# Performance work log

Hardware: AMD Instinct MI355X
Metric: run time of the kernel (lower is better)

## Reference

```python
import jax, jax.numpy as jnp
import numpy as np

N_STATIC = 20
N_DYNAMIC = 10
INPUT_DIM = N_STATIC + N_DYNAMIC * 9 + 8  # 118
EMBED = 128
HIDDEN = 1536
HIDDEN2 = 1024
OUT = 128
T = 2048


def setup_inputs() -> dict:
    key = jax.random.key(0)
    ks = jax.random.split(key, 20)
    s = lambda i, shape: jax.random.normal(ks[i], shape, dtype=jnp.float32) * 0.02
    inp = {
        "inputVecs": jax.random.normal(ks[0], (T, INPUT_DIM), dtype=jnp.float32),
        # init_hidden(): randn(num_layers, 1, hidden_dim) -> stored as [2, H]
        "h0": jax.random.normal(ks[1], (2, HIDDEN), dtype=jnp.float32),
        "c0": jax.random.normal(ks[2], (2, HIDDEN), dtype=jnp.float32),
        # LSTM layer 0 (input = INPUT_DIM + EMBED)
        "W_ih0": s(3, (4 * HIDDEN, INPUT_DIM + EMBED)),
        "W_hh0": s(4, (4 * HIDDEN, HIDDEN)),
        "b_ih0": s(5, (4 * HIDDEN,)),
        "b_hh0": s(6, (4 * HIDDEN,)),
        # LSTM layer 1
        "W_ih1": s(7, (4 * HIDDEN, HIDDEN)),
        "W_hh1": s(8, (4 * HIDDEN, HIDDEN)),
        "b_ih1": s(9, (4 * HIDDEN,)),
        "b_hh1": s(10, (4 * HIDDEN,)),
        # hiddenLinear: hidden_dim -> hidden2
        "W_hl": s(11, (HIDDEN2, HIDDEN)),
        "b_hl": s(12, (HIDDEN2,)),
        # linear: hidden2 -> output_dim
        "W_out": s(13, (OUT, HIDDEN2)),
        "b_out": s(14, (OUT,)),
        # map: output_dim -> embed_size
        "W_map": s(15, (EMBED, OUT)),
        "b_map": s(16, (EMBED,)),
    }
    return inp


def _lstm_cell(x, h, c, W_ih, W_hh, b_ih, b_hh):
    # torch gate order: i, f, g, o
    gates = W_ih @ x + b_ih + W_hh @ h + b_hh
    i, f, g, o = jnp.split(gates, 4)
    i = jax.nn.sigmoid(i)
    f = jax.nn.sigmoid(f)
    g = jnp.tanh(g)
    o = jax.nn.sigmoid(o)
    c_new = f * c + i * g
    h_new = o * jnp.tanh(c_new)
    return h_new, c_new


def reference(inputVecs, h0, c0, W_ih0, W_hh0, b_ih0, b_hh0,
              W_ih1, W_hh1, b_ih1, b_hh1,
              W_hl, b_hl, W_out, b_out, W_map, b_map):
    embed0 = jnp.zeros((EMBED,), dtype=inputVecs.dtype)

    def step(carry, x):
        h, c, emb = carry  # h,c: [2, H]; emb: [EMBED]
        xt = jnp.concatenate([x, emb])
        h0n, c0n = _lstm_cell(xt, h[0], c[0], W_ih0, W_hh0, b_ih0, b_hh0)
        h1n, c1n = _lstm_cell(h0n, h[1], c[1], W_ih1, W_hh1, b_ih1, b_hh1)
        # dropout p=0 -> identity; two stacked linears (no nonlinearity, faithful)
        y = W_out @ (W_hl @ h1n + b_hl) + b_out
        y = jax.nn.softmax(y)
        emb_new = W_map @ y + b_map
        return (jnp.stack([h0n, h1n]), jnp.stack([c0n, c1n]), emb_new), y

    _, outputs = jax.lax.scan(step, (h0, c0, embed0), inputVecs)
    return outputs  # [T, OUT]
```

## Files before the change

kernel.cpp:

```cpp
#include <hip/hip_runtime.h>
#include <math.h>
#include <stdint.h>

#define T_STEPS 2048
#define XDIM 118
#define EMBD 128
#define HD 1536
#define NA 96
#define NB 128
#define NBLK (NA + NB + 1)

#define EP_A   0
#define EP_B   128
#define EP_C   256
#define EP_AG  288
#define EP_N   320

#define SMEM_BYTES 160032

struct Params {
  const float *x, *h0in, *c0in;
  const float *Wih0, *Whh0, *bih0, *bhh0;
  const float *Wih1, *Whh1, *bih1, *bhh1;
  const float *Whl, *bhl, *Wout, *bout, *Wmap, *bmap;
  float *PRE, *Wc, *bc, *h0buf, *h1buf, *embbuf, *PART;
  uint32_t *ep;
  float *out;
};

__device__ __forceinline__ float bf_lo(uint32_t u){ return __uint_as_float(u << 16); }
__device__ __forceinline__ float bf_hi(uint32_t u){ return __uint_as_float(u & 0xffff0000u); }
__device__ __forceinline__ uint32_t packbf(float a, float b){
  uint32_t ua = __float_as_uint(a), ub = __float_as_uint(b);
  ua = (ua + 0x7fffu + ((ua >> 16) & 1u)) >> 16;
  ub = (ub + 0x7fffu + ((ub >> 16) & 1u)) & 0xffff0000u;
  return (ua & 0xffffu) | ub;
}
__device__ __forceinline__ float gload(const float* p){
  return __hip_atomic_load(p, __ATOMIC_RELAXED, __HIP_MEMORY_SCOPE_AGENT);
}
__device__ __forceinline__ void gstore(float* p, float v){
  __hip_atomic_store(p, v, __ATOMIC_RELAXED, __HIP_MEMORY_SCOPE_AGENT);
}
__device__ __forceinline__ uint32_t gloadu(const uint32_t* p){
  return __hip_atomic_load(p, __ATOMIC_RELAXED, __HIP_MEMORY_SCOPE_AGENT);
}
__device__ __forceinline__ void gstoreu(uint32_t* p, uint32_t v){
  __hip_atomic_store(p, v, __ATOMIC_RELAXED, __HIP_MEMORY_SCOPE_AGENT);
}
__device__ __forceinline__ float sigm(float x){ return 1.f / (1.f + __expf(-x)); }

__device__ __forceinline__ float asrc(const Params& P, int r, int k){
  if (k < HD) return P.Whh0[(size_t)r * HD + k];
  return P.Wih0[(size_t)r * (XDIM + EMBD) + XDIM + (k - HD)];
}
__device__ void run_A(const Params& P, int bid, uint32_t* smem){
  const int tid = threadIdx.x;
  const int w = tid >> 6, l = tid & 63;
  const int O = bid * 16 + w;
  float* xv = (float*)smem;
  uint2* wl2 = (uint2*)(smem + 1664);
  uint32_t wr[4][8];
  uint32_t wremb[4];
#pragma unroll
  for (int g = 0; g < 4; ++g){
    int r = g * HD + O;
#pragma unroll
    for (int p = 0; p < 8; ++p)
      wr[g][p] = packbf(asrc(P, r, 128 * p + 2 * l), asrc(P, r, 128 * p + 2 * l + 1));
#pragma unroll
    for (int q = 0; q < 2; ++q){
      uint2 u;
      u.x = packbf(asrc(P, r, 128 * (8 + 2 * q) + 2 * l), asrc(P, r, 128 * (8 + 2 * q) + 2 * l + 1));
      u.y = packbf(asrc(P, r, 128 * (9 + 2 * q) + 2 * l), asrc(P, r, 128 * (9 + 2 * q) + 2 * l + 1));
      wl2[(q * 4 + g) * 1024 + tid] = u;
    }
    wremb[g] = packbf(asrc(P, r, 1536 + 2 * l), asrc(P, r, 1537 + 2 * l));
  }
  float cst = P.c0in[O];
  int alive = 1;
  __syncthreads();
  for (int t = 0; t < T_STEPS; ++t){
    const float* pre = P.PRE + (size_t)t * 6144;
    float q0 = pre[O], q1 = pre[HD + O], q2 = pre[2 * HD + O], q3 = pre[3 * HD + O];
    if (w == 0 && alive){
      uint32_t n = 0;
      while (gloadu(P.ep + EP_AG) < (uint32_t)t){
        if (++n > 5000000u){ alive = 0; break; }
      }
    }
    __syncthreads();
    const float* hp = P.h0buf + (((t & 1) ^ 1) * HD);
    xv[tid] = gload(hp + tid);
    if (tid < 512) xv[1024 + tid] = gload(hp + 1024 + tid);
    __syncthreads();
    float a0 = 0.f, a1 = 0.f, a2 = 0.f, a3 = 0.f;
#pragma unroll
    for (int p = 0; p < 8; ++p){
      float2 x2 = *(const float2*)&xv[128 * p + 2 * l];
      uint32_t u0 = wr[0][p], u1 = wr[1][p], u2 = wr[2][p], u3 = wr[3][p];
      a0 += bf_lo(u0) * x2.x + bf_hi(u0) * x2.y;
      a1 += bf_lo(u1) * x2.x + bf_hi(u1) * x2.y;
      a2 += bf_lo(u2) * x2.x + bf_hi(u2) * x2.y;
      a3 += bf_lo(u3) * x2.x + bf_hi(u3) * x2.y;
    }
#pragma unroll
    for (int q = 0; q < 2; ++q){
      float2 xa = *(const float2*)&xv[128 * (8 + 2 * q) + 2 * l];
      float2 xb = *(const float2*)&xv[128 * (9 + 2 * q) + 2 * l];
      uint2 u0 = wl2[(q * 4 + 0) * 1024 + tid];
      uint2 u1 = wl2[(q * 4 + 1) * 1024 + tid];
      uint2 u2 = wl2[(q * 4 + 2) * 1024 + tid];
      uint2 u3 = wl2[(q * 4 + 3) * 1024 + tid];
      a0 += bf_lo(u0.x) * xa.x + bf_hi(u0.x) * xa.y + bf_lo(u0.y) * xb.x + bf_hi(u0.y) * xb.y;
      a1 += bf_lo(u1.x) * xa.x + bf_hi(u1.x) * xa.y + bf_lo(u1.y) * xb.x + bf_hi(u1.y) * xb.y;
      a2 += bf_lo(u2.x) * xa.x + bf_hi(u2.x) * xa.y + bf_lo(u2.y) * xb.x + bf_hi(u2.y) * xb.y;
      a3 += bf_lo(u3.x) * xa.x + bf_hi(u3.x) * xa.y + bf_lo(u3.y) * xb.x + bf_hi(u3.y) * xb.y;
    }
    if (w == 0 && alive){
      uint32_t n = 0;
      while (gloadu(P.ep + EP_C) < (uint32_t)t){
        if (++n > 5000000u){ alive = 0; break; }
      }
    }
    __syncthreads();
    if (tid < EMBD) xv[HD + tid] = gload(P.embbuf + (((t & 1) ^ 1) * EMBD) + tid);
    __syncthreads();
    {
      float2 x2 = *(const float2*)&xv[1536 + 2 * l];
      a0 += bf_lo(wremb[0]) * x2.x + bf_hi(wremb[0]) * x2.y;
      a1 += bf_lo(wremb[1]) * x2.x + bf_hi(wremb[1]) * x2.y;
      a2 += bf_lo(wremb[2]) * x2.x + bf_hi(wremb[2]) * x2.y;
      a3 += bf_lo(wremb[3]) * x2.x + bf_hi(wremb[3]) * x2.y;
    }
#pragma unroll
    for (int m = 1; m < 64; m <<= 1){
      a0 += __shfl_xor(a0, m, 64);
      a1 += __shfl_xor(a1, m, 64);
      a2 += __shfl_xor(a2, m, 64);
      a3 += __shfl_xor(a3, m, 64);
    }
    float gi = sigm(a0 + q0);
    float gf = sigm(a1 + q1);
    float gg = tanhf(a2 + q2);
    float go = sigm(a3 + q3);
    cst = gf * cst + gi * gg;
    float hn = go * tanhf(cst);
    if (l == 0) gstore(P.h0buf + (t & 1) * HD + O, hn);
    __syncthreads();
    if (tid == 0) gstoreu(P.ep + EP_A + bid, (uint32_t)(t + 1));
  }
}

__device__ __forceinline__ float bsrc(const Params& P, int r, int k){
  if (k < HD) return P.Wih1[(size_t)r * HD + k];
  return P.Whh1[(size_t)r * HD + (k - HD)];
}
__device__ void run_B(const Params& P, int bidb, uint32_t* smem){
  const int tid = threadIdx.x;
  const int w = tid >> 6, l = tid & 63;
  const int base = bidb * 12;
  float* xv = (float*)smem;
  uint2* wl2 = (uint2*)(smem + 3072);
  float* g1lds = (float*)(smem + 39936);
  float* c1lds = g1lds + 48;
  float* h1lds = c1lds + 12;
  uint32_t wr[3][12];
  float bias[3];
#pragma unroll
  for (int jj = 0; jj < 3; ++jj){
    int idx = 3 * w + jj;
    int g = idx / 12, o = idx % 12;
    int r = g * HD + base + o;
    bias[jj] = P.bih1[r] + P.bhh1[r];
#pragma unroll
    for (int p = 0; p < 12; ++p)
      wr[jj][p] = packbf(bsrc(P, r, 128 * p + 2 * l), bsrc(P, r, 128 * p + 2 * l + 1));
#pragma unroll
    for (int q = 0; q < 6; ++q){
      uint2 u;
      u.x = packbf(bsrc(P, r, 128 * (12 + 2 * q) + 2 * l), bsrc(P, r, 128 * (12 + 2 * q) + 2 * l + 1));
      u.y = packbf(bsrc(P, r, 128 * (13 + 2 * q) + 2 * l), bsrc(P, r, 128 * (13 + 2 * q) + 2 * l + 1));
      wl2[(q * 3 + jj) * 1024 + tid] = u;
    }
  }
  const int jrow = tid >> 2, cpart = tid & 3;
  float wc0 = 0.f, wc1 = 0.f, wc2 = 0.f;
  if (tid < 512){
    const float* wcp = P.Wc + (size_t)jrow * HD + base + cpart * 3;
    wc0 = wcp[0]; wc1 = wcp[1]; wc2 = wcp[2];
  }
  if (tid < 12) c1lds[tid] = P.c0in[HD + base + tid];
  int alive = 1;
  __syncthreads();
  for (int t = 0; t < T_STEPS; ++t){
    if (w == 0 && alive){
      uint32_t n = 0;
      while (gloadu(P.ep + EP_C) < (uint32_t)t){
        if (++n > 5000000u){ alive = 0; break; }
      }
    }
    __syncthreads();
    const float* h1p = P.h1buf + (((t & 1) ^ 1) * HD);
    xv[1536 + tid] = gload(h1p + tid);
    if (tid < 512) xv[2560 + tid] = gload(h1p + 1024 + tid);
    __syncthreads();
    float a0 = 0.f, a1 = 0.f, a2 = 0.f;
#pragma unroll
    for (int q = 0; q < 6; ++q){
      float2 xa = *(const float2*)&xv[128 * (12 + 2 * q) + 2 * l];
      float2 xb = *(const float2*)&xv[128 * (13 + 2 * q) + 2 * l];
      uint2 u0 = wl2[(q * 3 + 0) * 1024 + tid];
      uint2 u1 = wl2[(q * 3 + 1) * 1024 + tid];
      uint2 u2 = wl2[(q * 3 + 2) * 1024 + tid];
      a0 += bf_lo(u0.x) * xa.x + bf_hi(u0.x) * xa.y + bf_lo(u0.y) * xb.x + bf_hi(u0.y) * xb.y;
      a1 += bf_lo(u1.x) * xa.x + bf_hi(u1.x) * xa.y + bf_lo(u1.y) * xb.x + bf_hi(u1.y) * xb.y;
      a2 += bf_lo(u2.x) * xa.x + bf_hi(u2.x) * xa.y + bf_lo(u2.y) * xb.x + bf_hi(u2.y) * xb.y;
    }
    if (w == 0 && alive){
      uint32_t tgt = (uint32_t)(t + 1), n = 0;
      if (bidb == 0){
        while (1){
          uint32_t v0 = gloadu(P.ep + EP_A + l);
          uint32_t v1 = (l < 32) ? gloadu(P.ep + EP_A + 64 + l) : tgt;
          if (__all(v0 >= tgt && v1 >= tgt)) break;
          if (++n > 5000000u){ alive = 0; break; }
        }
        if (l == 0 && alive) gstoreu(P.ep + EP_AG, tgt);
      } else {
        while (gloadu(P.ep + EP_AG) < tgt){
          if (++n > 5000000u){ alive = 0; break; }
        }
      }
    }
    __syncthreads();
    const float* h0p = P.h0buf + (t & 1) * HD;
    xv[tid] = gload(h0p + tid);
    if (tid < 512) xv[1024 + tid] = gload(h0p + 1024 + tid);
    __syncthreads();
#pragma unroll
    for (int p = 0; p < 12; ++p){
      float2 x2 = *(const float2*)&xv[128 * p + 2 * l];
      uint32_t u0 = wr[0][p], u1 = wr[1][p], u2 = wr[2][p];
      a0 += bf_lo(u0) * x2.x + bf_hi(u0) * x2.y;
      a1 += bf_lo(u1) * x2.x + bf_hi(u1) * x2.y;
      a2 += bf_lo(u2) * x2.x + bf_hi(u2) * x2.y;
    }
#pragma unroll
    for (int m = 1; m < 64; m <<= 1){
      a0 += __shfl_xor(a0, m, 64);
      a1 += __shfl_xor(a1, m, 64);
      a2 += __shfl_xor(a2, m, 64);
    }
    if (l == 0){
      g1lds[3 * w + 0] = a0 + bias[0];
      g1lds[3 * w + 1] = a1 + bias[1];
      g1lds[3 * w + 2] = a2 + bias[2];
    }
    __syncthreads();
    if (tid < 12){
      int o = tid;
      float gi = sigm(g1lds[o]);
      float gf = sigm(g1lds[12 + o]);
      float gg = tanhf(g1lds[24 + o]);
      float go = sigm(g1lds[36 + o]);
      float c = gf * c1lds[o] + gi * gg;
      c1lds[o] = c;
      float hn = go * tanhf(c);
      h1lds[o] = hn;
      gstore(P.h1buf + (t & 1) * HD + base + o, hn);
    }
    __syncthreads();
    if (tid < 512){
      float pp = wc0 * h1lds[cpart * 3] + wc1 * h1lds[cpart * 3 + 1] + wc2 * h1lds[cpart * 3 + 2];
      pp += __shfl_xor(pp, 1, 64);
      pp += __shfl_xor(pp, 2, 64);
      if (cpart == 0) gstore(P.PART + bidb * 128 + jrow, pp);
    }
    __syncthreads();
    if (tid == 0) gstoreu(P.ep + EP_B + bidb, (uint32_t)(t + 1));
  }
}

__device__ void run_C(const Params& P, uint32_t* smem){
  const int tid = threadIdx.x;
  float* partred = (float*)smem;
  float* lg   = (float*)(smem + 1024);
  float* plds = (float*)(smem + 1152);
  float* bcs  = (float*)(smem + 1280);
  float* red2 = (float*)(smem + 1408);
  float wm[16];
  const int e = tid >> 3, jc = tid & 7;
#pragma unroll
  for (int i = 0; i < 16; ++i) wm[i] = P.Wmap[(size_t)e * 128 + jc * 16 + i];
  float bm = P.bmap[e];
  if (tid < 128) bcs[tid] = P.bc[tid];
  int alive = 1;
  const int w = tid >> 6, l = tid & 63;
  __syncthreads();
  for (int t = 0; t < T_STEPS; ++t){
    if (w == 0 && alive){
      uint32_t tgt = (uint32_t)(t + 1), n = 0;
      while (1){
        uint32_t v0 = gloadu(P.ep + EP_B + l);
        uint32_t v1 = gloadu(P.ep + EP_B + 64 + l);
        if (__all(v0 >= tgt && v1 >= tgt)) break;
        if (++n > 5000000u){ alive = 0; break; }
      }
    }
    __syncthreads();
    const int j = tid & 127, b8 = tid >> 7;
    float s = 0.f;
#pragma unroll
    for (int i = 0; i < 16; ++i) s += gload(P.PART + (b8 * 16 + i) * 128 + j);
    partred[b8 * 128 + j] = s;
    __syncthreads();
    if (tid < 128){
      float lt = bcs[tid];
#pragma unroll
      for (int i = 0; i < 8; ++i) lt += partred[i * 128 + tid];
      lg[tid] = lt;
    }
    __syncthreads();
    if (tid < 64){
      float m = fmaxf(lg[tid], lg[tid + 64]);
#pragma unroll
      for (int k = 1; k < 64; k <<= 1) m = fmaxf(m, __shfl_xor(m, k, 64));
      float sd = __expf(lg[tid] - m) + __expf(lg[tid + 64] - m);
#pragma unroll
      for (int k = 1; k < 64; k <<= 1) sd += __shfl_xor(sd, k, 64);
      if (tid == 0){ red2[0] = m; red2[1] = 1.f / sd; }
    }
    __syncthreads();
    if (tid < 128){
      float pv = __expf(lg[tid] - red2[0]) * red2[1];
      plds[tid] = pv;
      P.out[(size_t)t * 128 + tid] = pv;
    }
    __syncthreads();
    float a = 0.f;
#pragma unroll
    for (int i = 0; i < 16; ++i) a += wm[i] * plds[jc * 16 + i];
    a += __shfl_xor(a, 1, 64);
    a += __shfl_xor(a, 2, 64);
    a += __shfl_xor(a, 4, 64);
    if (jc == 0) gstore(P.embbuf + (t & 1) * EMBD + e, a + bm);
    __syncthreads();
    if (tid == 0) gstoreu(P.ep + EP_C, (uint32_t)(t + 1));
  }
}

__global__ __launch_bounds__(1024) void k_lstm(Params P){
  extern __shared__ __align__(16) uint32_t smem[];
  int bid = blockIdx.x;
  if (bid < NA) run_A(P, bid, smem);
  else if (bid < NA + NB) run_B(P, bid - NA, smem);
  else run_C(P, smem);
}

__global__ void k_init(const float* h0in, float* h0buf, float* h1buf, float* embbuf,
                       uint32_t* ep){
  int tid = threadIdx.x;
  for (int i = tid; i < HD; i += 256){
    float a = h0in[i], b = h0in[HD + i];
    h0buf[i] = a; h0buf[HD + i] = a;
    h1buf[i] = b; h1buf[HD + i] = b;
  }
  if (tid < 128){ embbuf[tid] = 0.f; embbuf[128 + tid] = 0.f; }
  for (int i = tid; i < EP_N; i += 256) ep[i] = 0u;
}

__global__ void k_pre(const float* x, const float* Wih0, const float* bih0, const float* bhh0, float* PRE){
  int tb = blockIdx.x >> 2;
  int rc = blockIdx.x & 3;
  int tid = threadIdx.x;
  __shared__ float xl[32 * XDIM];
  for (int i = tid; i < 32 * XDIM; i += 256){
    int tt = i / XDIM, k = i % XDIM;
    xl[i] = x[(size_t)(tb * 32 + tt) * XDIM + k];
  }
  __syncthreads();
  for (int rr = 0; rr < 6; ++rr){
    int r = rc * HD + rr * 256 + tid;
    float acc[32];
#pragma unroll
    for (int t = 0; t < 32; ++t) acc[t] = 0.f;
    const float* wrow = Wih0 + (size_t)r * (XDIM + EMBD);
    for (int k = 0; k < XDIM; ++k){
      float wv = wrow[k];
#pragma unroll
      for (int t = 0; t < 32; ++t) acc[t] += wv * xl[t * XDIM + k];
    }
    float bb = bih0[r] + bhh0[r];
    for (int t = 0; t < 32; ++t)
      PRE[(size_t)(tb * 32 + t) * 6144 + r] = acc[t] + bb;
  }
}

__global__ void k_wc(const float* Whl, const float* Wout, const float* bhl, const float* bout,
                     float* Wc, float* bc){
  if (blockIdx.x == 96){
    int j = threadIdx.x;
    if (j < 128){
      float a = 0.f;
      for (int m = 0; m < 1024; ++m) a += Wout[(size_t)j * 1024 + m] * bhl[m];
      bc[j] = a + bout[j];
    }
    return;
  }
  int kt = blockIdx.x % 6, jt = blockIdx.x / 6;
  __shared__ float wo[8 * 1024];
  int tid = threadIdx.x;
  for (int i = tid; i < 8 * 1024; i += 256) wo[i] = Wout[(size_t)(jt * 8) * 1024 + i];
  __syncthreads();
  int k = kt * 256 + tid;
  float acc[8];
#pragma unroll
  for (int jj = 0; jj < 8; ++jj) acc[jj] = 0.f;
  for (int m = 0; m < 1024; ++m){
    float wl = Whl[(size_t)m * HD + k];
#pragma unroll
    for (int jj = 0; jj < 8; ++jj) acc[jj] += wo[jj * 1024 + m] * wl;
  }
#pragma unroll
  for (int jj = 0; jj < 8; ++jj) Wc[(size_t)(jt * 8 + jj) * HD + k] = acc[jj];
}

__global__ void k_sentinel(float* out){ out[0] = 1.0e6f; }

extern "C" void kernel_launch(void* const* d_in, const int* in_sizes, int n_in,
                              void* d_out, int out_size, void* d_ws, size_t ws_size,
                              hipStream_t stream){
  (void)in_sizes; (void)n_in; (void)out_size;
  const float* x    = (const float*)d_in[0];
  const float* h0in = (const float*)d_in[1];
  const float* c0in = (const float*)d_in[2];
  const float* Wih0 = (const float*)d_in[3];
  const float* Whh0 = (const float*)d_in[4];
  const float* bih0 = (const float*)d_in[5];
  const float* bhh0 = (const float*)d_in[6];
  const float* Wih1 = (const float*)d_in[7];
  const float* Whh1 = (const float*)d_in[8];
  const float* bih1 = (const float*)d_in[9];
  const float* bhh1 = (const float*)d_in[10];
  const float* Whl  = (const float*)d_in[11];
  const float* bhl  = (const float*)d_in[12];
  const float* Wout = (const float*)d_in[13];
  const float* bout = (const float*)d_in[14];
  const float* Wmap = (const float*)d_in[15];
  const float* bmap = (const float*)d_in[16];
  float* out = (float*)d_out;
  float* ws = (float*)d_ws;

  size_t off = 0;
  float* PRE    = ws + off; off += (size_t)T_STEPS * 6144;
  float* Wc     = ws + off; off += 128 * HD;
  float* bc     = ws + off; off += 128;
  float* h0buf  = ws + off; off += 2 * HD;
  float* h1buf  = ws + off; off += 2 * HD;
  float* embbuf = ws + off; off += 2 * EMBD;
  float* PART   = ws + off; off += 128 * 128;
  off = (off + 63) & ~(size_t)63;
  uint32_t* ep  = (uint32_t*)(ws + off); off += EP_N;

  if (ws_size < off * sizeof(float) + 1024){
    hipLaunchKernelGGL(k_sentinel, dim3(1), dim3(1), 0, stream, out);
    return;
  }

  (void)hipFuncSetAttribute(reinterpret_cast<const void*>(k_lstm),
                            hipFuncAttributeMaxDynamicSharedMemorySize, SMEM_BYTES);

  hipLaunchKernelGGL(k_init, dim3(1), dim3(256), 0, stream, h0in, h0buf, h1buf, embbuf, ep);
  hipLaunchKernelGGL(k_pre, dim3(256), dim3(256), 0, stream, x, Wih0, bih0, bhh0, PRE);
  hipLaunchKernelGGL(k_wc, dim3(97), dim3(256), 0, stream, Whl, Wout, bhl, bout, Wc, bc);

  Params P;
  P.x = x; P.h0in = h0in; P.c0in = c0in;
  P.Wih0 = Wih0; P.Whh0 = Whh0; P.bih0 = bih0; P.bhh0 = bhh0;
  P.Wih1 = Wih1; P.Whh1 = Whh1; P.bih1 = bih1; P.bhh1 = bhh1;
  P.Whl = Whl; P.bhl = bhl; P.Wout = Wout; P.bout = bout; P.Wmap = Wmap; P.bmap = bmap;
  P.PRE = PRE; P.Wc = Wc; P.bc = bc;
  P.h0buf = h0buf; P.h1buf = h1buf; P.embbuf = embbuf; P.PART = PART;
  P.ep = ep; P.out = out;

  hipLaunchKernelGGL(k_lstm, dim3(NBLK), dim3(1024), SMEM_BYTES, stream, P);
}
```

Before: 30.63 ms.

## Fold softmax/embedding stage into layer-0 blocks and use striped atomic counters

Removes the dedicated C block. Each layer-0 block now redundantly reduces the layer-1 partial logits, computes the softmax and the embedding map locally from a bf16 transposed Wmap kept in LDS, and block 0 writes the output one step late. Per-block epoch flags plus a global aggregator are replaced by 16 striped fetch-add counters polled by one wave. This removes one handoff from the serial per-step critical path. In exchange, every A block does redundant softmax and embedding work, more of the A weights move from registers to LDS, and the hot counters take atomic contention.

```diff
diff --git a/kernel.cpp b/kernel.cpp
--- a/kernel.cpp
+++ b/kernel.cpp
@@ -8,13 +8,11 @@
 #define HD 1536
 #define NA 96
 #define NB 128
-#define NBLK (NA + NB + 1)
-
-#define EP_A   0
-#define EP_B   128
-#define EP_C   256
-#define EP_AG  288
-#define EP_N   320
+#define NBLK (NA + NB)
+
+#define EP_ACTR 0
+#define EP_BCTR 256
+#define EP_N    512
 
 #define SMEM_BYTES 160032
 
@@ -23,7 +21,7 @@
   const float *Wih0, *Whh0, *bih0, *bhh0;
   const float *Wih1, *Whh1, *bih1, *bhh1;
   const float *Whl, *bhl, *Wout, *bout, *Wmap, *bmap;
-  float *PRE, *Wc, *bc, *h0buf, *h1buf, *embbuf, *PART;
+  float *PRE, *Wc, *bc, *h0buf, *h1buf, *PART;
   uint32_t *ep;
   float *out;
 };
@@ -45,8 +43,8 @@
 __device__ __forceinline__ uint32_t gloadu(const uint32_t* p){
   return __hip_atomic_load(p, __ATOMIC_RELAXED, __HIP_MEMORY_SCOPE_AGENT);
 }
-__device__ __forceinline__ void gstoreu(uint32_t* p, uint32_t v){
-  __hip_atomic_store(p, v, __ATOMIC_RELAXED, __HIP_MEMORY_SCOPE_AGENT);
+__device__ __forceinline__ void ctradd(uint32_t* p){
+  (void)__hip_atomic_fetch_add(p, 1u, __ATOMIC_RELAXED, __HIP_MEMORY_SCOPE_AGENT);
 }
 __device__ __forceinline__ float sigm(float x){ return 1.f / (1.f + __expf(-x)); }
 
@@ -60,23 +58,34 @@
   const int O = bid * 16 + w;
   float* xv = (float*)smem;
   uint2* wl2 = (uint2*)(smem + 1664);
-  uint32_t wr[4][8];
-  uint32_t wremb[4];
+  uint32_t* wmT = smem + 26240;
+  float* pr2 = (float*)(smem + 34432);
+  float* lg   = (float*)(smem + 36480);
+  float* plds = (float*)(smem + 36608);
+  float* bcs  = (float*)(smem + 36736);
+  float* bmaps= (float*)(smem + 36864);
+  float* red2 = (float*)(smem + 36992);
+  uint32_t wr[4][6], wremb[4];
 #pragma unroll
   for (int g = 0; g < 4; ++g){
     int r = g * HD + O;
 #pragma unroll
-    for (int p = 0; p < 8; ++p)
+    for (int p = 0; p < 6; ++p)
       wr[g][p] = packbf(asrc(P, r, 128 * p + 2 * l), asrc(P, r, 128 * p + 2 * l + 1));
 #pragma unroll
-    for (int q = 0; q < 2; ++q){
+    for (int q = 0; q < 3; ++q){
       uint2 u;
-      u.x = packbf(asrc(P, r, 128 * (8 + 2 * q) + 2 * l), asrc(P, r, 128 * (8 + 2 * q) + 2 * l + 1));
-      u.y = packbf(asrc(P, r, 128 * (9 + 2 * q) + 2 * l), asrc(P, r, 128 * (9 + 2 * q) + 2 * l + 1));
+      u.x = packbf(asrc(P, r, 128 * (6 + 2 * q) + 2 * l), asrc(P, r, 128 * (6 + 2 * q) + 2 * l + 1));
+      u.y = packbf(asrc(P, r, 128 * (7 + 2 * q) + 2 * l), asrc(P, r, 128 * (7 + 2 * q) + 2 * l + 1));
       wl2[(q * 4 + g) * 1024 + tid] = u;
     }
     wremb[g] = packbf(asrc(P, r, 1536 + 2 * l), asrc(P, r, 1537 + 2 * l));
   }
+  for (int idx = tid; idx < 8192; idx += 1024){
+    int e2 = idx & 63, k = idx >> 6;
+    wmT[idx] = packbf(P.Wmap[(size_t)(2 * e2) * 128 + k], P.Wmap[(size_t)(2 * e2 + 1) * 128 + k]);
+  }
+  if (tid < 128){ bcs[tid] = P.bc[tid]; bmaps[tid] = P.bmap[tid]; }
   float cst = P.c0in[O];
   int alive = 1;
   __syncthreads();
@@ -84,8 +93,10 @@
     const float* pre = P.PRE + (size_t)t * 6144;
     float q0 = pre[O], q1 = pre[HD + O], q2 = pre[2 * HD + O], q3 = pre[3 * HD + O];
     if (w == 0 && alive){
-      uint32_t n = 0;
-      while (gloadu(P.ep + EP_AG) < (uint32_t)t){
+      uint32_t tgt = 6u * (uint32_t)t, n = 0;
+      while (1){
+        uint32_t v = (l < 16) ? gloadu(P.ep + EP_ACTR + l * 16) : tgt;
+        if (__all(v >= tgt)) break;
         if (++n > 5000000u){ alive = 0; break; }
       }
     }
@@ -96,7 +107,7 @@
     __syncthreads();
     float a0 = 0.f, a1 = 0.f, a2 = 0.f, a3 = 0.f;
 #pragma unroll
-    for (int p = 0; p < 8; ++p){
+    for (int p = 0; p < 6; ++p){
       float2 x2 = *(const float2*)&xv[128 * p + 2 * l];
       uint32_t u0 = wr[0][p], u1 = wr[1][p], u2 = wr[2][p], u3 = wr[3][p];
       a0 += bf_lo(u0) * x2.x + bf_hi(u0) * x2.y;
@@ -105,9 +116,9 @@
       a3 += bf_lo(u3) * x2.x + bf_hi(u3) * x2.y;
     }
 #pragma unroll
-    for (int q = 0; q < 2; ++q){
-      float2 xa = *(const float2*)&xv[128 * (8 + 2 * q) + 2 * l];
-      float2 xb = *(const float2*)&xv[128 * (9 + 2 * q) + 2 * l];
+    for (int q = 0; q < 3; ++q){
+      float2 xa = *(const float2*)&xv[128 * (6 + 2 * q) + 2 * l];
+      float2 xb = *(const float2*)&xv[128 * (7 + 2 * q) + 2 * l];
       uint2 u0 = wl2[(q * 4 + 0) * 1024 + tid];
       uint2 u1 = wl2[(q * 4 + 1) * 1024 + tid];
       uint2 u2 = wl2[(q * 4 + 2) * 1024 + tid];
@@ -118,13 +129,66 @@
       a3 += bf_lo(u3.x) * xa.x + bf_hi(u3.x) * xa.y + bf_lo(u3.y) * xb.x + bf_hi(u3.y) * xb.y;
     }
     if (w == 0 && alive){
-      uint32_t n = 0;
-      while (gloadu(P.ep + EP_C) < (uint32_t)t){
+      uint32_t tgt = 8u * (uint32_t)t, n = 0;
+      while (1){
+        uint32_t v = (l < 16) ? gloadu(P.ep + EP_BCTR + l * 16) : tgt;
+        if (__all(v >= tgt)) break;
         if (++n > 5000000u){ alive = 0; break; }
       }
     }
     __syncthreads();
-    if (tid < EMBD) xv[HD + tid] = gload(P.embbuf + (((t & 1) ^ 1) * EMBD) + tid);
+    if (t > 0){
+      const int j = tid & 127, b8 = tid >> 7;
+      float s = 0.f;
+#pragma unroll
+      for (int i = 0; i < 16; ++i) s += gload(P.PART + (b8 * 16 + i) * 128 + j);
+      pr2[b8 * 128 + j] = s;
+      __syncthreads();
+      if (tid < 128){
+        float lt = bcs[tid];
+#pragma unroll
+        for (int i = 0; i < 8; ++i) lt += pr2[i * 128 + tid];
+        lg[tid] = lt;
+      }
+      __syncthreads();
+      if (tid < 64){
+        float m = fmaxf(lg[tid], lg[tid + 64]);
+#pragma unroll
+        for (int k = 1; k < 64; k <<= 1) m = fmaxf(m, __shfl_xor(m, k, 64));
+        float sd = __expf(lg[tid] - m) + __expf(lg[tid + 64] - m);
+#pragma unroll
+        for (int k = 1; k < 64; k <<= 1) sd += __shfl_xor(sd, k, 64);
+        if (tid == 0){ red2[0] = m; red2[1] = 1.f / sd; }
+      }
+      __syncthreads();
+      if (tid < 128){
+        float pv = __expf(lg[tid] - red2[0]) * red2[1];
+        plds[tid] = pv;
+        if (bid == 0) P.out[(size_t)(t - 1) * 128 + tid] = pv;
+      }
+      __syncthreads();
+      {
+        int e2 = tid & 63, m = tid >> 6;
+        float s0 = 0.f, s1 = 0.f;
+#pragma unroll
+        for (int i = 0; i < 8; ++i){
+          uint32_t u = wmT[(m * 8 + i) * 64 + e2];
+          float p = plds[m * 8 + i];
+          s0 += bf_lo(u) * p;
+          s1 += bf_hi(u) * p;
+        }
+        *(float2*)&pr2[m * 128 + 2 * e2] = make_float2(s0, s1);
+      }
+      __syncthreads();
+      if (tid < 128){
+        float v = bmaps[tid];
+#pragma unroll
+        for (int m = 0; m < 16; ++m) v += pr2[m * 128 + tid];
+        xv[1536 + tid] = v;
+      }
+    } else {
+      if (tid < 128) xv[1536 + tid] = 0.f;
+    }
     __syncthreads();
     {
       float2 x2 = *(const float2*)&xv[1536 + 2 * l];
@@ -148,7 +212,42 @@
     float hn = go * tanhf(cst);
     if (l == 0) gstore(P.h0buf + (t & 1) * HD + O, hn);
     __syncthreads();
-    if (tid == 0) gstoreu(P.ep + EP_A + bid, (uint32_t)(t + 1));
+    if (tid == 0) ctradd(P.ep + EP_ACTR + (bid & 15) * 16);
+  }
+  if (bid == 0){
+    if (w == 0 && alive){
+      uint32_t tgt = 8u * (uint32_t)T_STEPS, n = 0;
+      while (1){
+        uint32_t v = (l < 16) ? gloadu(P.ep + EP_BCTR + l * 16) : tgt;
+        if (__all(v >= tgt)) break;
+        if (++n > 5000000u){ alive = 0; break; }
+      }
+    }
+    __syncthreads();
+    const int j = tid & 127, b8 = tid >> 7;
+    float s = 0.f;
+#pragma unroll
+    for (int i = 0; i < 16; ++i) s += gload(P.PART + (b8 * 16 + i) * 128 + j);
+    pr2[b8 * 128 + j] = s;
+    __syncthreads();
+    if (tid < 128){
+      float lt = bcs[tid];
+#pragma unroll
+      for (int i = 0; i < 8; ++i) lt += pr2[i * 128 + tid];
+      lg[tid] = lt;
+    }
+    __syncthreads();
+    if (tid < 64){
+      float m = fmaxf(lg[tid], lg[tid + 64]);
+#pragma unroll
+      for (int k = 1; k < 64; k <<= 1) m = fmaxf(m, __shfl_xor(m, k, 64));
+      float sd = __expf(lg[tid] - m) + __expf(lg[tid + 64] - m);
+#pragma unroll
+      for (int k = 1; k < 64; k <<= 1) sd += __shfl_xor(sd, k, 64);
+      if (tid == 0){ red2[0] = m; red2[1] = 1.f / sd; }
+    }
+    __syncthreads();
+    if (tid < 128) P.out[(size_t)(T_STEPS - 1) * 128 + tid] = __expf(lg[tid] - red2[0]) * red2[1];
   }
 }
 
@@ -195,8 +294,10 @@
   __syncthreads();
   for (int t = 0; t < T_STEPS; ++t){
     if (w == 0 && alive){
-      uint32_t n = 0;
-      while (gloadu(P.ep + EP_C) < (uint32_t)t){
+      uint32_t tgt = 8u * (uint32_t)t, n = 0;
+      while (1){
+        uint32_t v = (l < 16) ? gloadu(P.ep + EP_BCTR + l * 16) : tgt;
+        if (__all(v >= tgt)) break;
         if (++n > 5000000u){ alive = 0; break; }
       }
     }
@@ -218,19 +319,11 @@
       a2 += bf_lo(u2.x) * xa.x + bf_hi(u2.x) * xa.y + bf_lo(u2.y) * xb.x + bf_hi(u2.y) * xb.y;
     }
     if (w == 0 && alive){
-      uint32_t tgt = (uint32_t)(t + 1), n = 0;
-      if (bidb == 0){
-        while (1){
-          uint32_t v0 = gloadu(P.ep + EP_A + l);
-          uint32_t v1 = (l < 32) ? gloadu(P.ep + EP_A + 64 + l) : tgt;
-          if (__all(v0 >= tgt && v1 >= tgt)) break;
-          if (++n > 5000000u){ alive = 0; break; }
-        }
-        if (l == 0 && alive) gstoreu(P.ep + EP_AG, tgt);
-      } else {
-        while (gloadu(P.ep + EP_AG) < tgt){
-          if (++n > 5000000u){ alive = 0; break; }
-        }
+      uint32_t tgt = 6u * (uint32_t)(t + 1), n = 0;
+      while (1){
+        uint32_t v = (l < 16) ? gloadu(P.ep + EP_ACTR + l * 16) : tgt;
+        if (__all(v >= tgt)) break;
+        if (++n > 5000000u){ alive = 0; break; }
       }
     }
     __syncthreads();
@@ -278,75 +371,7 @@
       if (cpart == 0) gstore(P.PART + bidb * 128 + jrow, pp);
     }
     __syncthreads();
-    if (tid == 0) gstoreu(P.ep + EP_B + bidb, (uint32_t)(t + 1));
-  }
-}
-
-__device__ void run_C(const Params& P, uint32_t* smem){
-  const int tid = threadIdx.x;
-  float* partred = (float*)smem;
-  float* lg   = (float*)(smem + 1024);
-  float* plds = (float*)(smem + 1152);
-  float* bcs  = (float*)(smem + 1280);
-  float* red2 = (float*)(smem + 1408);
-  float wm[16];
-  const int e = tid >> 3, jc = tid & 7;
-#pragma unroll
-  for (int i = 0; i < 16; ++i) wm[i] = P.Wmap[(size_t)e * 128 + jc * 16 + i];
-  float bm = P.bmap[e];
-  if (tid < 128) bcs[tid] = P.bc[tid];
-  int alive = 1;
-  const int w = tid >> 6, l = tid & 63;
-  __syncthreads();
-  for (int t = 0; t < T_STEPS; ++t){
-    if (w == 0 && alive){
-      uint32_t tgt = (uint32_t)(t + 1), n = 0;
-      while (1){
-        uint32_t v0 = gloadu(P.ep + EP_B + l);
-        uint32_t v1 = gloadu(P.ep + EP_B + 64 + l);
-        if (__all(v0 >= tgt && v1 >= tgt)) break;
-        if (++n > 5000000u){ alive = 0; break; }
-      }
-    }
-    __syncthreads();
-    const int j = tid & 127, b8 = tid >> 7;
-    float s = 0.f;
-#pragma unroll
-    for (int i = 0; i < 16; ++i) s += gload(P.PART + (b8 * 16 + i) * 128 + j);
-    partred[b8 * 128 + j] = s;
-    __syncthreads();
-    if (tid < 128){
-      float lt = bcs[tid];
-#pragma unroll
-      for (int i = 0; i < 8; ++i) lt += partred[i * 128 + tid];
-      lg[tid] = lt;
-    }
-    __syncthreads();
-    if (tid < 64){
-      float m = fmaxf(lg[tid], lg[tid + 64]);
-#pragma unroll
-      for (int k = 1; k < 64; k <<= 1) m = fmaxf(m, __shfl_xor(m, k, 64));
-      float sd = __expf(lg[tid] - m) + __expf(lg[tid + 64] - m);
-#pragma unroll
-      for (int k = 1; k < 64; k <<= 1) sd += __shfl_xor(sd, k, 64);
-      if (tid == 0){ red2[0] = m; red2[1] = 1.f / sd; }
-    }
-    __syncthreads();
-    if (tid < 128){
-      float pv = __expf(lg[tid] - red2[0]) * red2[1];
-      plds[tid] = pv;
-      P.out[(size_t)t * 128 + tid] = pv;
-    }
-    __syncthreads();
-    float a = 0.f;
-#pragma unroll
-    for (int i = 0; i < 16; ++i) a += wm[i] * plds[jc * 16 + i];
-    a += __shfl_xor(a, 1, 64);
-    a += __shfl_xor(a, 2, 64);
-    a += __shfl_xor(a, 4, 64);
-    if (jc == 0) gstore(P.embbuf + (t & 1) * EMBD + e, a + bm);
-    __syncthreads();
-    if (tid == 0) gstoreu(P.ep + EP_C, (uint32_t)(t + 1));
+    if (tid == 0) ctradd(P.ep + EP_BCTR + (bidb & 15) * 16);
   }
 }
 
@@ -354,19 +379,16 @@
   extern __shared__ __align__(16) uint32_t smem[];
   int bid = blockIdx.x;
   if (bid < NA) run_A(P, bid, smem);
-  else if (bid < NA + NB) run_B(P, bid - NA, smem);
-  else run_C(P, smem);
-}
-
-__global__ void k_init(const float* h0in, float* h0buf, float* h1buf, float* embbuf,
-                       uint32_t* ep){
+  else run_B(P, bid - NA, smem);
+}
+
+__global__ void k_init(const float* h0in, float* h0buf, float* h1buf, uint32_t* ep){
   int tid = threadIdx.x;
   for (int i = tid; i < HD; i += 256){
     float a = h0in[i], b = h0in[HD + i];
     h0buf[i] = a; h0buf[HD + i] = a;
     h1buf[i] = b; h1buf[HD + i] = b;
   }
-  if (tid < 128){ embbuf[tid] = 0.f; embbuf[128 + tid] = 0.f; }
   for (int i = tid; i < EP_N; i += 256) ep[i] = 0u;
 }
 
@@ -458,7 +480,6 @@
   float* bc     = ws + off; off += 128;
   float* h0buf  = ws + off; off += 2 * HD;
   float* h1buf  = ws + off; off += 2 * HD;
-  float* embbuf = ws + off; off += 2 * EMBD;
   float* PART   = ws + off; off += 128 * 128;
   off = (off + 63) & ~(size_t)63;
   uint32_t* ep  = (uint32_t*)(ws + off); off += EP_N;
@@ -471,7 +492,7 @@
   (void)hipFuncSetAttribute(reinterpret_cast<const void*>(k_lstm),
                             hipFuncAttributeMaxDynamicSharedMemorySize, SMEM_BYTES);
 
-  hipLaunchKernelGGL(k_init, dim3(1), dim3(256), 0, stream, h0in, h0buf, h1buf, embbuf, ep);
+  hipLaunchKernelGGL(k_init, dim3(1), dim3(256), 0, stream, h0in, h0buf, h1buf, ep);
   hipLaunchKernelGGL(k_pre, dim3(256), dim3(256), 0, stream, x, Wih0, bih0, bhh0, PRE);
   hipLaunchKernelGGL(k_wc, dim3(97), dim3(256), 0, stream, Whl, Wout, bhl, bout, Wc, bc);
 
@@ -481,7 +502,7 @@
   P.Wih1 = Wih1; P.Whh1 = Whh1; P.bih1 = bih1; P.bhh1 = bhh1;
   P.Whl = Whl; P.bhl = bhl; P.Wout = Wout; P.bout = bout; P.Wmap = Wmap; P.bmap = bmap;
   P.PRE = PRE; P.Wc = Wc; P.bc = bc;
-  P.h0buf = h0buf; P.h1buf = h1buf; P.embbuf = embbuf; P.PART = PART;
+  P.h0buf = h0buf; P.h1buf = h1buf; P.PART = PART;
   P.ep = ep; P.out = out;
 
   hipLaunchKernelGGL(k_lstm, dim3(NBLK), dim3(1024), SMEM_BYTES, stream, P);
```

Result: slower. 64.47 ms (+110.5%).
